# Kernel tuning notes

Hardware: AMD Instinct MI355X
Metric: run time of the kernel (lower is better)

Reference implementation:

```python
import jax, jax.numpy as jnp
import numpy as np

EMB = 1024   # emb_dim
HID = 1024   # hid_dim (must equal EMB for the original router to be well-formed)
E = 16       # num_experts
K = 2        # num_active_experts


def setup_inputs() -> dict:
    key = jax.random.key(0)
    ks = jax.random.split(key, 5)
    s_in = (2.0 / EMB) ** 0.5
    s_hid = (2.0 / HID) ** 0.5
    x = jax.random.normal(ks[0], (2, 4096, EMB), dtype=jnp.float32)
    w_gate = jax.random.normal(ks[1], (EMB, E), dtype=jnp.float32) * s_in
    w1 = jax.random.normal(ks[2], (E, EMB, HID), dtype=jnp.float32) * s_in  # exp_1 weights
    w2 = jax.random.normal(ks[3], (E, EMB, HID), dtype=jnp.float32) * s_in  # exp_2 weights
    wc = jax.random.normal(ks[4], (E, HID, EMB), dtype=jnp.float32) * s_hid  # contr weights
    return {"x": x, "w_gate": w_gate, "w1": w1, "w2": w2, "wc": wc}


def reference(x, w_gate, w1, w2, wc):
    b, s, d = x.shape
    xf = x.reshape(-1, d)                      # [N, d]
    n = xf.shape[0]
    # Router: softmax over expert logits, then top-k (no renormalization of topk scores,
    # matching the torch module).
    probs = jax.nn.softmax(xf @ w_gate, axis=-1)   # [N, E]
    scores, idx = jax.lax.top_k(probs, K)          # [N, K]
    # Dense gate matrix: gate[t, e] = score if e in topk(t) else 0 (topk indices distinct).
    gates = jnp.zeros((n, E), dtype=xf.dtype).at[jnp.arange(n)[:, None], idx].set(scores)
    # Loop (scan) over the fixed expert count; each expert runs a SwiGLU MLP over all
    # tokens and its output is combined with the (mostly zero) gate weights. This is the
    # standard dense-combine MoE reference: same math as the masked torch loop since
    # unselected tokens get gate 0.
    def body(acc, ws):
        w1e, w2e, wce, ge = ws                 # [d,h], [d,h], [h,d], [N]
        h = jax.nn.silu(xf @ w1e) * (xf @ w2e)  # [N, h]
        return acc + ge[:, None] * (h @ wce), None

    out, _ = jax.lax.scan(body, jnp.zeros_like(xf), (w1, w2, wc, gates.T))
    return out.reshape(b, s, d)
```

## Files before the change

kernel.cpp:

```cpp
#include <hip/hip_runtime.h>
#include <hip/hip_bf16.h>
#include <stdint.h>

#define EMB 1024
#define HID 1024
#define NE 16
#define NTOK 8192
#define NSLOT (NTOK * 2)
#define BM 128
#define BN 128
#define BK 32

typedef __bf16 bf16;
typedef __bf16 bf16x8 __attribute__((ext_vector_type(8)));
typedef __bf16 bf16x4 __attribute__((ext_vector_type(4)));
typedef float f32x4 __attribute__((ext_vector_type(4)));

#define GLOAD16(g, l)                                                        \
  __builtin_amdgcn_global_load_lds(                                          \
      (const __attribute__((address_space(1))) void*)(g),                    \
      (__attribute__((address_space(3))) void*)(l), 16, 0, 0)

__global__ void transpose_cvt3(const float* __restrict__ w1, const float* __restrict__ w2,
                               const float* __restrict__ wcs, bf16* __restrict__ w1t,
                               bf16* __restrict__ w2t, bf16* __restrict__ wct) {
  __shared__ float tile[32][33];
  int zz = blockIdx.z;
  const float* s; bf16* d;
  if (zz < 16)      { s = w1;  d = w1t; }
  else if (zz < 32) { s = w2;  d = w2t; }
  else              { s = wcs; d = wct; }
  int z = zz & 15;
  int x0 = blockIdx.x << 5, y0 = blockIdx.y << 5;
  s += (size_t)z * EMB * HID;
  d += (size_t)z * EMB * HID;
  int tx = threadIdx.x, ty = threadIdx.y;
#pragma unroll
  for (int i = 0; i < 32; i += 8)
    tile[ty + i][tx] = s[(size_t)(y0 + ty + i) * 1024 + x0 + tx];
  __syncthreads();
#pragma unroll
  for (int i = 0; i < 32; i += 8)
    d[(size_t)(x0 + ty + i) * 1024 + y0 + tx] = (bf16)tile[tx][ty + i];
}

__global__ void wgT_k(const float* __restrict__ wg, float* __restrict__ wgT) {
  int f = blockIdx.x * 256 + threadIdx.x;
  int d = f >> 4, e = f & 15;
  wgT[e * 1024 + d] = wg[f];
}

__launch_bounds__(1024)
__global__ void router_k(const float* __restrict__ x, const float* __restrict__ wgT,
                         bf16* __restrict__ xb,
                         int* __restrict__ tokexp, float* __restrict__ tokgate) {
  __shared__ float wgs[NE * 1024];
  for (int i = threadIdx.x; i < 4096; i += 1024)
    ((float4*)wgs)[i] = ((const float4*)wgT)[i];
  __syncthreads();

  int t = blockIdx.x * 16 + (threadIdx.x >> 6);
  int lane = threadIdx.x & 63;
  const float* xr = x + (size_t)t * EMB;

  float acc[NE];
#pragma unroll
  for (int e = 0; e < NE; e++) acc[e] = 0.f;

#pragma unroll
  for (int c = 0; c < 4; c++) {
    float4 xv = ((const float4*)xr)[c * 64 + lane];
    int dbase = c * 256 + lane * 4;
    bf16x4 o;
    o[0] = (bf16)xv.x; o[1] = (bf16)xv.y; o[2] = (bf16)xv.z; o[3] = (bf16)xv.w;
    *(bf16x4*)(xb + (size_t)t * EMB + dbase) = o;
#pragma unroll
    for (int e = 0; e < NE; e++) {
      float4 wv = *(const float4*)&wgs[e * 1024 + dbase];
      acc[e] += xv.x * wv.x + xv.y * wv.y + xv.z * wv.z + xv.w * wv.w;
    }
  }
#pragma unroll
  for (int e = 0; e < NE; e++) {
#pragma unroll
    for (int s = 32; s > 0; s >>= 1) acc[e] += __shfl_xor(acc[e], s);
  }
  if (lane == 0) {
    float m = acc[0];
#pragma unroll
    for (int e = 1; e < NE; e++) m = fmaxf(m, acc[e]);
    float p[NE]; float sum = 0.f;
#pragma unroll
    for (int e = 0; e < NE; e++) { p[e] = __expf(acc[e] - m); sum += p[e]; }
    float inv = 1.f / sum;
#pragma unroll
    for (int e = 0; e < NE; e++) p[e] *= inv;
    int i1 = 0;
#pragma unroll
    for (int e = 1; e < NE; e++) if (p[e] > p[i1]) i1 = e;
    int i2 = (i1 == 0) ? 1 : 0;
#pragma unroll
    for (int e = 0; e < NE; e++) if (e != i1 && p[e] > p[i2]) i2 = e;
    tokexp[2 * t] = i1; tokexp[2 * t + 1] = i2;
    tokgate[2 * t] = p[i1]; tokgate[2 * t + 1] = p[i2];
  }
}

__global__ void hist_k(const int* __restrict__ tokexp, int* __restrict__ blockcnt) {
  __shared__ int h[NE];
  int tid = threadIdx.x;
  if (tid < NE) h[tid] = 0;
  __syncthreads();
  int e = tokexp[blockIdx.x * 256 + tid];
  atomicAdd(&h[e], 1);
  __syncthreads();
  if (tid < NE) blockcnt[blockIdx.x * NE + tid] = h[tid];
}

__global__ void scan_k(const int* __restrict__ blockcnt, int* __restrict__ cnt,
                       int* __restrict__ eoff, int* __restrict__ blockoff) {
  __shared__ int scnt[NE], soff[NE];
  int t = threadIdx.x;
  if (t < NE) {
    int s = 0;
    for (int b = 0; b < 64; b++) s += blockcnt[b * NE + t];
    scnt[t] = s;
    cnt[t] = s;
  }
  __syncthreads();
  if (t == 0) {
    int s = 0;
    for (int e = 0; e < NE; e++) { soff[e] = s; eoff[e] = s; s += scnt[e]; }
  }
  __syncthreads();
  if (t < NE) {
    int run = soff[t];
    for (int b = 0; b < 64; b++) { blockoff[b * NE + t] = run; run += blockcnt[b * NE + t]; }
  }
}

__global__ void assign_k(const int* __restrict__ tokexp, const float* __restrict__ tokgate,
                         const int* __restrict__ blockoff, int* __restrict__ rowtok,
                         float* __restrict__ rowgate) {
  __shared__ int wavecnt[4][NE];
  __shared__ int waveoff[4][NE];
  int tid = threadIdx.x;
  int w = tid >> 6, lane = tid & 63;
  int s = blockIdx.x * 256 + tid;
  int e = tokexp[s];
  int rank = 0;
  unsigned long long ltmask = (1ull << lane) - 1ull;
#pragma unroll
  for (int ee = 0; ee < NE; ee++) {
    unsigned long long bal = __ballot(e == ee);
    if (e == ee) rank = __popcll(bal & ltmask);
    if (lane == ee) wavecnt[w][ee] = __popcll(bal);
  }
  __syncthreads();
  if (tid < 64) {
    int ww = tid >> 4, ee = tid & 15;
    int off = 0;
    for (int p = 0; p < ww; p++) off += wavecnt[p][ee];
    waveoff[ww][ee] = off;
  }
  __syncthreads();
  int pos = blockoff[blockIdx.x * NE + e] + waveoff[w][e] + rank;
  rowtok[pos] = s >> 1;
  rowgate[pos] = tokgate[s];
}

__launch_bounds__(256, 2)
__global__ void gemm1_k(const bf16* __restrict__ xb, const bf16* __restrict__ w1t,
                        const bf16* __restrict__ w2t, const int* __restrict__ cnt,
                        const int* __restrict__ eoff, const int* __restrict__ rowtok,
                        bf16* __restrict__ H) {
  int id = blockIdx.x;
  int nid = (id & 7) * 1024 + (id >> 3);
  int e = nid >> 9;
  int rem = nid & 511;
  int m0 = (rem >> 3) * BM;
  int n0 = (rem & 7) * BN;
  int n_e = cnt[e];
  if (m0 >= n_e) return;
  int base = eoff[e];

  __shared__ __align__(16) bf16 sA[BM * BK];
  __shared__ __align__(16) bf16 sB1[BN * BK];
  __shared__ __align__(16) bf16 sB2[BN * BK];

  int tid = threadIdx.x;
  int lane = tid & 63;
  int w = tid >> 6;
  int wr = (w >> 1) << 6;
  int wc = (w & 1) << 6;

  int srow = tid >> 2;
  int kc = (tid & 3) << 3;

  const bf16* ag[2];
#pragma unroll
  for (int i = 0; i < 2; i++) {
    int gi = base + m0 + (i << 6) + srow;
    gi = gi < NSLOT ? gi : NSLOT - 1;
    ag[i] = xb + (size_t)rowtok[gi] * EMB + kc;
  }
  const bf16* b1g = w1t + ((size_t)e * HID + n0 + srow) * EMB + kc;
  const bf16* b2g = w2t + ((size_t)e * HID + n0 + srow) * EMB + kc;

  char* lA = (char*)sA + w * 1024;
  char* lB1 = (char*)sB1 + w * 1024;
  char* lB2 = (char*)sB2 + w * 1024;

  f32x4 acc1[4][4] = {};
  f32x4 acc2[4][4] = {};

  int ra = (wr + (lane & 15)) * BK + ((lane >> 4) << 3);
  int rb = (wc + (lane & 15)) * BK + ((lane >> 4) << 3);

  for (int k0 = 0; k0 < EMB; k0 += BK) {
    GLOAD16(ag[0] + k0, lA);
    GLOAD16(ag[1] + k0, lA + 4096);
    GLOAD16(b1g + k0, lB1);
    GLOAD16(b1g + (size_t)64 * EMB + k0, lB1 + 4096);
    GLOAD16(b2g + k0, lB2);
    GLOAD16(b2g + (size_t)64 * EMB + k0, lB2 + 4096);
    __syncthreads();

    bf16x8 af[4], b1f[4], b2f[4];
#pragma unroll
    for (int m = 0; m < 4; m++) af[m] = *(const bf16x8*)&sA[ra + m * 16 * BK];
#pragma unroll
    for (int n = 0; n < 4; n++) {
      b1f[n] = *(const bf16x8*)&sB1[rb + n * 16 * BK];
      b2f[n] = *(const bf16x8*)&sB2[rb + n * 16 * BK];
    }
#pragma unroll
    for (int m = 0; m < 4; m++)
#pragma unroll
      for (int n = 0; n < 4; n++) {
        acc1[m][n] = __builtin_amdgcn_mfma_f32_16x16x32_bf16(af[m], b1f[n], acc1[m][n], 0, 0, 0);
        acc2[m][n] = __builtin_amdgcn_mfma_f32_16x16x32_bf16(af[m], b2f[n], acc2[m][n], 0, 0, 0);
      }
    __syncthreads();
  }

  int rf = wr + ((lane >> 4) << 2);
  int cf = n0 + wc + (lane & 15);
#pragma unroll
  for (int m = 0; m < 4; m++) {
#pragma unroll
    for (int n = 0; n < 4; n++) {
#pragma unroll
      for (int b = 0; b < 4; b++) {
        int gr = m0 + rf + m * 16 + b;
        if (gr < n_e) {
          float c1 = acc1[m][n][b];
          float c2 = acc2[m][n][b];
          float h = c1 * c2 / (1.f + __expf(-c1));
          H[(size_t)(base + gr) * HID + cf + n * 16] = (bf16)h;
        }
      }
    }
  }
}

__launch_bounds__(256, 2)
__global__ void gemm2_k(const bf16* __restrict__ H, const bf16* __restrict__ wct,
                        const int* __restrict__ cnt, const int* __restrict__ eoff,
                        const int* __restrict__ rowtok, const float* __restrict__ rowgate,
                        float* __restrict__ out) {
  int id = blockIdx.x;
  int nid = (id & 7) * 1024 + (id >> 3);
  int e = nid >> 9;
  int rem = nid & 511;
  int m0 = (rem >> 3) * BM;
  int n0 = (rem & 7) * BN;
  int n_e = cnt[e];
  if (m0 >= n_e) return;
  int base = eoff[e];

  __shared__ __align__(16) bf16 sA[BM * BK];
  __shared__ __align__(16) bf16 sB[BN * BK];

  int tid = threadIdx.x;
  int lane = tid & 63;
  int w = tid >> 6;
  int wr = (w >> 1) << 6;
  int wc = (w & 1) << 6;

  int srow = tid >> 2;
  int kc = (tid & 3) << 3;

  const bf16* ag[2];
#pragma unroll
  for (int i = 0; i < 2; i++) {
    int gi = base + m0 + (i << 6) + srow;
    gi = gi < NSLOT ? gi : NSLOT - 1;
    ag[i] = H + (size_t)gi * HID + kc;
  }
  const bf16* bg = wct + ((size_t)e * EMB + n0 + srow) * HID + kc;

  char* lA = (char*)sA + w * 1024;
  char* lB = (char*)sB + w * 1024;

  f32x4 acc[4][4] = {};

  int ra = (wr + (lane & 15)) * BK + ((lane >> 4) << 3);
  int rb = (wc + (lane & 15)) * BK + ((lane >> 4) << 3);

  for (int k0 = 0; k0 < HID; k0 += BK) {
    GLOAD16(ag[0] + k0, lA);
    GLOAD16(ag[1] + k0, lA + 4096);
    GLOAD16(bg + k0, lB);
    GLOAD16(bg + (size_t)64 * HID + k0, lB + 4096);
    __syncthreads();

    bf16x8 af[4], bfr[4];
#pragma unroll
    for (int m = 0; m < 4; m++) af[m] = *(const bf16x8*)&sA[ra + m * 16 * BK];
#pragma unroll
    for (int n = 0; n < 4; n++) bfr[n] = *(const bf16x8*)&sB[rb + n * 16 * BK];
#pragma unroll
    for (int m = 0; m < 4; m++)
#pragma unroll
      for (int n = 0; n < 4; n++)
        acc[m][n] = __builtin_amdgcn_mfma_f32_16x16x32_bf16(af[m], bfr[n], acc[m][n], 0, 0, 0);
    __syncthreads();
  }

  int rf = wr + ((lane >> 4) << 2);
  int cf = n0 + wc + (lane & 15);
#pragma unroll
  for (int m = 0; m < 4; m++) {
#pragma unroll
    for (int b = 0; b < 4; b++) {
      int gr = m0 + rf + m * 16 + b;
      if (gr < n_e) {
        int idx = base + gr;
        int tok = rowtok[idx];
        float g = rowgate[idx];
        float* orow = out + (size_t)tok * EMB + cf;
#pragma unroll
        for (int n = 0; n < 4; n++)
          atomicAdd(orow + n * 16, g * acc[m][n][b]);
      }
    }
  }
}

extern "C" void kernel_launch(void* const* d_in, const int* in_sizes, int n_in,
                              void* d_out, int out_size, void* d_ws, size_t ws_size,
                              hipStream_t stream) {
  const float* x  = (const float*)d_in[0];
  const float* wg = (const float*)d_in[1];
  const float* w1 = (const float*)d_in[2];
  const float* w2 = (const float*)d_in[3];
  const float* wc = (const float*)d_in[4];
  float* out = (float*)d_out;

  const size_t WELEM = (size_t)NE * EMB * HID;
  bf16* w1t  = (bf16*)d_ws;
  bf16* w2t  = w1t + WELEM;
  bf16* wct  = w2t + WELEM;
  bf16* xb   = wct + WELEM;
  bf16* Hbuf = xb + (size_t)NTOK * EMB;
  int* cnt      = (int*)(Hbuf + (size_t)NSLOT * HID);
  int* eoff     = cnt + 16;
  int* blockcnt = eoff + 16;
  int* blockoff = blockcnt + 64 * 16;
  int* tokexp   = blockoff + 64 * 16;
  float* tokgate = (float*)(tokexp + NSLOT);
  int* rowtok    = (int*)(tokgate + NSLOT);
  float* rowgate = (float*)(rowtok + NSLOT);
  float* wgT     = rowgate + NSLOT;

  hipMemsetAsync(out, 0, (size_t)out_size * sizeof(float), stream);

  dim3 tb(32, 8), tg(32, 32, 48);
  transpose_cvt3<<<tg, tb, 0, stream>>>(w1, w2, wc, w1t, w2t, wct);
  wgT_k<<<64, 256, 0, stream>>>(wg, wgT);
  router_k<<<NTOK / 16, 1024, 0, stream>>>(x, wgT, xb, tokexp, tokgate);
  hist_k<<<NSLOT / 256, 256, 0, stream>>>(tokexp, blockcnt);
  scan_k<<<1, 64, 0, stream>>>(blockcnt, cnt, eoff, blockoff);
  assign_k<<<NSLOT / 256, 256, 0, stream>>>(tokexp, tokgate, blockoff, rowtok, rowgate);
  gemm1_k<<<8192, 256, 0, stream>>>(xb, w1t, w2t, cnt, eoff, rowtok, Hbuf);
  gemm2_k<<<8192, 256, 0, stream>>>(Hbuf, wct, cnt, eoff, rowtok, rowgate, out);
}
```

Baseline: 308.9 us.

## Rewrite expert GEMMs with 256x256 tiles, double-buffered pipelining and interleaved gate/up weights

Both expert GEMMs move to 512-thread blocks with 256x256 output tiles and BK=64. K-tiles are double-buffered in 128KB of dynamic LDS with an XOR-swizzled layout, and the loop uses explicit vmcnt waits, barriers and setprio phases to overlap global loads with MFMA work. W1 and W2 are interleaved row-wise into one concatenated weight, so a single accumulator set yields both projections, and SwiGLU is formed by exchanging neighbouring lanes with a shuffle. gemm2 adds a 2-way split-K, relying on the existing atomic adds. The transpose/convert kernel is rewritten with 64x64 tiles and vectorized bf16 stores. The larger tiles cut redundant weight and activation traffic, but they waste more work on partially filled expert tiles, lower occupancy, and double the atomic traffic in gemm2.

Result: slower. 363.4 us (+17.6%).

```diff
diff --git a/kernel.cpp b/kernel.cpp
--- a/kernel.cpp
+++ b/kernel.cpp
@@ -7,9 +7,6 @@
 #define NE 16
 #define NTOK 8192
 #define NSLOT (NTOK * 2)
-#define BM 128
-#define BN 128
-#define BK 32
 
 typedef __bf16 bf16;
 typedef __bf16 bf16x8 __attribute__((ext_vector_type(8)));
@@ -21,27 +18,103 @@
       (const __attribute__((address_space(1))) void*)(g),                    \
       (__attribute__((address_space(3))) void*)(l), 16, 0, 0)
 
+
+#define VMW(N) asm volatile("s_waitcnt vmcnt(" #N ")" ::: "memory")
+#define NOPS ((void)0)
+
+#define PH_PRE                                                \
+  __builtin_amdgcn_s_barrier();                               \
+  asm volatile("s_waitcnt lgkmcnt(0)" ::: "memory");          \
+  __builtin_amdgcn_sched_barrier(0);                          \
+  __builtin_amdgcn_s_setprio(1)
+#define PH_POST                                               \
+  __builtin_amdgcn_s_setprio(0);                              \
+  __builtin_amdgcn_s_barrier()
+
+#define LDA(D, M, CK) (*(const bf16x8*)&sh[((((D)<<1) + wm) << 13) + l15 * 64 + (CK) + (M) * 1024])
+#define LDB(D, N, CK) (*(const bf16x8*)&sh[32768 + ((((D)<<1) + (wn >> 1)) << 13) + ((wn & 1) << 12) + l15 * 64 + (CK) + (N) * 1024])
+
+#define STG_A(D, KO) do {                                                     \
+    GLOAD16(agp00 + (KO), (char*)sh + ((((D)<<1) + 0) << 14) + wb);           \
+    GLOAD16(agp01 + (KO), (char*)sh + ((((D)<<1) + 0) << 14) + 8192 + wb);    \
+    GLOAD16(agp10 + (KO), (char*)sh + ((((D)<<1) + 1) << 14) + wb);           \
+    GLOAD16(agp11 + (KO), (char*)sh + ((((D)<<1) + 1) << 14) + 8192 + wb);    \
+  } while (0)
+#define STG_B(D, KO) do {                                                     \
+    GLOAD16(bgp00 + (KO), (char*)sh + 65536 + ((((D)<<1) + 0) << 14) + wb);   \
+    GLOAD16(bgp01 + (KO), (char*)sh + 65536 + ((((D)<<1) + 0) << 14) + 8192 + wb); \
+    GLOAD16(bgp10 + (KO), (char*)sh + 65536 + ((((D)<<1) + 1) << 14) + wb);   \
+    GLOAD16(bgp11 + (KO), (char*)sh + 65536 + ((((D)<<1) + 1) << 14) + 8192 + wb); \
+  } while (0)
+
+#define MM(MB, FA, FB) do {                                                   \
+    _Pragma("unroll") for (int mq = 0; mq < 4; mq++)                          \
+    _Pragma("unroll") for (int nq = 0; nq < 4; nq++)                          \
+      acc[(MB) + mq][nq] = __builtin_amdgcn_mfma_f32_16x16x32_bf16(           \
+          FA[mq], FB[nq], acc[(MB) + mq][nq], 0, 0, 0);                       \
+  } while (0)
+
+#define KTILE(D, S3, S4, W4) do {                                             \
+    bf16x8 fa[4], fb[4], g0[4], g1[4];                                        \
+    _Pragma("unroll") for (int q = 0; q < 4; q++) g0[q] = LDB(D, q, c0);      \
+    _Pragma("unroll") for (int q = 0; q < 4; q++) fa[q] = LDA(D, q, c0);      \
+    PH_PRE; MM(0, fa, g0); PH_POST;                                           \
+    _Pragma("unroll") for (int q = 0; q < 4; q++) fb[q] = LDA(D, 4 + q, c0);  \
+    _Pragma("unroll") for (int q = 0; q < 4; q++) g1[q] = LDB(D, q, c1);      \
+    PH_PRE; MM(4, fb, g0); PH_POST;                                           \
+    _Pragma("unroll") for (int q = 0; q < 4; q++) fa[q] = LDA(D, q, c1);      \
+    _Pragma("unroll") for (int q = 0; q < 4; q++) fb[q] = LDA(D, 4 + q, c1);  \
+    S3;                                                                       \
+    PH_PRE; MM(0, fa, g1); PH_POST;                                           \
+    S4; W4;                                                                   \
+    PH_PRE; MM(4, fb, g1); PH_POST;                                           \
+  } while (0)
+
+#define KLOOP(NT2) do {                                                       \
+    STG_A(0, 0); STG_B(0, 0); STG_A(1, 64); STG_B(1, 64);                     \
+    VMW(8); __builtin_amdgcn_s_barrier();                                     \
+    _Pragma("unroll 1") for (int i = 0; i < (NT2) - 1; i++) {                 \
+      int k2 = (i * 2 + 2) * 64, k3 = (i * 2 + 3) * 64;                       \
+      KTILE(0, STG_B(0, k2), STG_A(0, k2), VMW(6));                           \
+      KTILE(1, STG_B(1, k3), STG_A(1, k3), VMW(6));                           \
+    }                                                                         \
+    KTILE(0, NOPS, NOPS, VMW(0));                                             \
+    KTILE(1, NOPS, NOPS, NOPS);                                               \
+  } while (0)
+
 __global__ void transpose_cvt3(const float* __restrict__ w1, const float* __restrict__ w2,
-                               const float* __restrict__ wcs, bf16* __restrict__ w1t,
-                               bf16* __restrict__ w2t, bf16* __restrict__ wct) {
-  __shared__ float tile[32][33];
+                               const float* __restrict__ wcs, bf16* __restrict__ wcat,
+                               bf16* __restrict__ wct) {
+  __shared__ bf16 tile[64][68];
   int zz = blockIdx.z;
-  const float* s; bf16* d;
-  if (zz < 16)      { s = w1;  d = w1t; }
-  else if (zz < 32) { s = w2;  d = w2t; }
-  else              { s = wcs; d = wct; }
-  int z = zz & 15;
-  int x0 = blockIdx.x << 5, y0 = blockIdx.y << 5;
-  s += (size_t)z * EMB * HID;
-  d += (size_t)z * EMB * HID;
-  int tx = threadIdx.x, ty = threadIdx.y;
-#pragma unroll
-  for (int i = 0; i < 32; i += 8)
-    tile[ty + i][tx] = s[(size_t)(y0 + ty + i) * 1024 + x0 + tx];
-  __syncthreads();
-#pragma unroll
-  for (int i = 0; i < 32; i += 8)
-    d[(size_t)(x0 + ty + i) * 1024 + y0 + tx] = (bf16)tile[tx][ty + i];
+  const float* s; bf16* d; int mul, add;
+  if (zz < 16)      { s = w1 + ((size_t)zz << 20);        d = wcat + ((size_t)zz << 21);        mul = 2; add = 0; }
+  else if (zz < 32) { s = w2 + ((size_t)(zz - 16) << 20); d = wcat + ((size_t)(zz - 16) << 21); mul = 2; add = 1; }
+  else              { s = wcs + ((size_t)(zz - 32) << 20); d = wct + ((size_t)(zz - 32) << 20); mul = 1; add = 0; }
+  int k0 = blockIdx.y << 6, n0 = blockIdx.x << 6;
+  int t = threadIdx.x;
+
+  int r = t >> 4, c4 = t & 15;
+#pragma unroll
+  for (int i = 0; i < 4; i++) {
+    int row = r + (i << 4);
+    float4 v = *(const float4*)&s[(size_t)(k0 + row) * 1024 + n0 + (c4 << 2)];
+    bf16x4 o;
+    o[0] = (bf16)v.x; o[1] = (bf16)v.y; o[2] = (bf16)v.z; o[3] = (bf16)v.w;
+    *(bf16x4*)&tile[row][c4 << 2] = o;
+  }
+  __syncthreads();
+
+  int r8 = t >> 3, ch = t & 7;
+#pragma unroll
+  for (int i = 0; i < 2; i++) {
+    int on = r8 + (i << 5);
+    bf16x8 v;
+#pragma unroll
+    for (int j = 0; j < 8; j++) v[j] = tile[(ch << 3) + j][on];
+    int orow = (n0 + on) * mul + add;
+    *(bf16x8*)&d[(size_t)orow * 1024 + k0 + (ch << 3)] = v;
+  }
 }
 
 __global__ void wgT_k(const float* __restrict__ wg, float* __restrict__ wgT) {
@@ -169,183 +242,126 @@
   rowgate[pos] = tokgate[s];
 }
 
-__launch_bounds__(256, 2)
-__global__ void gemm1_k(const bf16* __restrict__ xb, const bf16* __restrict__ w1t,
-                        const bf16* __restrict__ w2t, const int* __restrict__ cnt,
-                        const int* __restrict__ eoff, const int* __restrict__ rowtok,
-                        bf16* __restrict__ H) {
+__launch_bounds__(512, 2)
+__global__ void gemm1_k(const bf16* __restrict__ xb, const bf16* __restrict__ wcat,
+                        const int* __restrict__ cnt, const int* __restrict__ eoff,
+                        const int* __restrict__ rowtok, bf16* __restrict__ Hb) {
   int id = blockIdx.x;
-  int nid = (id & 7) * 1024 + (id >> 3);
-  int e = nid >> 9;
-  int rem = nid & 511;
-  int m0 = (rem >> 3) * BM;
-  int n0 = (rem & 7) * BN;
+  int nid = (id & 7) * 512 + (id >> 3);
+  int e = nid >> 8, rem = nid & 255;
+  int m0 = (rem >> 3) << 8, n0 = (rem & 7) << 8;
   int n_e = cnt[e];
   if (m0 >= n_e) return;
-  int base = eoff[e];
-
-  __shared__ __align__(16) bf16 sA[BM * BK];
-  __shared__ __align__(16) bf16 sB1[BN * BK];
-  __shared__ __align__(16) bf16 sB2[BN * BK];
-
-  int tid = threadIdx.x;
-  int lane = tid & 63;
-  int w = tid >> 6;
-  int wr = (w >> 1) << 6;
-  int wc = (w & 1) << 6;
-
-  int srow = tid >> 2;
-  int kc = (tid & 3) << 3;
-
-  const bf16* ag[2];
-#pragma unroll
-  for (int i = 0; i < 2; i++) {
-    int gi = base + m0 + (i << 6) + srow;
-    gi = gi < NSLOT ? gi : NSLOT - 1;
-    ag[i] = xb + (size_t)rowtok[gi] * EMB + kc;
-  }
-  const bf16* b1g = w1t + ((size_t)e * HID + n0 + srow) * EMB + kc;
-  const bf16* b2g = w2t + ((size_t)e * HID + n0 + srow) * EMB + kc;
-
-  char* lA = (char*)sA + w * 1024;
-  char* lB1 = (char*)sB1 + w * 1024;
-  char* lB2 = (char*)sB2 + w * 1024;
-
-  f32x4 acc1[4][4] = {};
-  f32x4 acc2[4][4] = {};
-
-  int ra = (wr + (lane & 15)) * BK + ((lane >> 4) << 3);
-  int rb = (wc + (lane & 15)) * BK + ((lane >> 4) << 3);
-
-  for (int k0 = 0; k0 < EMB; k0 += BK) {
-    GLOAD16(ag[0] + k0, lA);
-    GLOAD16(ag[1] + k0, lA + 4096);
-    GLOAD16(b1g + k0, lB1);
-    GLOAD16(b1g + (size_t)64 * EMB + k0, lB1 + 4096);
-    GLOAD16(b2g + k0, lB2);
-    GLOAD16(b2g + (size_t)64 * EMB + k0, lB2 + 4096);
-    __syncthreads();
-
-    bf16x8 af[4], b1f[4], b2f[4];
-#pragma unroll
-    for (int m = 0; m < 4; m++) af[m] = *(const bf16x8*)&sA[ra + m * 16 * BK];
-#pragma unroll
-    for (int n = 0; n < 4; n++) {
-      b1f[n] = *(const bf16x8*)&sB1[rb + n * 16 * BK];
-      b2f[n] = *(const bf16x8*)&sB2[rb + n * 16 * BK];
-    }
-#pragma unroll
-    for (int m = 0; m < 4; m++)
-#pragma unroll
-      for (int n = 0; n < 4; n++) {
-        acc1[m][n] = __builtin_amdgcn_mfma_f32_16x16x32_bf16(af[m], b1f[n], acc1[m][n], 0, 0, 0);
-        acc2[m][n] = __builtin_amdgcn_mfma_f32_16x16x32_bf16(af[m], b2f[n], acc2[m][n], 0, 0, 0);
-      }
-    __syncthreads();
-  }
-
-  int rf = wr + ((lane >> 4) << 2);
-  int cf = n0 + wc + (lane & 15);
-#pragma unroll
-  for (int m = 0; m < 4; m++) {
-#pragma unroll
-    for (int n = 0; n < 4; n++) {
+  int base0 = eoff[e];
+  extern __shared__ bf16 sh[];
+
+  int tid = threadIdx.x, lane = tid & 63, w = tid >> 6;
+  int wm = w >> 2, wn = w & 3;
+  int l15 = lane & 15, l4 = lane >> 4, r7 = l15 & 7;
+  int c0 = ((l4 ^ r7) << 3), c1 = (((4 + l4) ^ r7) << 3);
+  int srow = tid >> 3;
+  int kg8 = (((tid & 7) ^ (srow & 7)) << 3);
+  int wb = w << 10;
+
+  const bf16 *agp00, *agp01, *agp10, *agp11, *bgp00, *bgp01, *bgp10, *bgp11;
+  {
+    int g0 = base0 + m0 + srow;        g0 = g0 < NSLOT ? g0 : NSLOT - 1;
+    int g1 = base0 + m0 + 64 + srow;   g1 = g1 < NSLOT ? g1 : NSLOT - 1;
+    int g2 = base0 + m0 + 128 + srow;  g2 = g2 < NSLOT ? g2 : NSLOT - 1;
+    int g3 = base0 + m0 + 192 + srow;  g3 = g3 < NSLOT ? g3 : NSLOT - 1;
+    agp00 = xb + ((size_t)rowtok[g0] << 10) + kg8;
+    agp01 = xb + ((size_t)rowtok[g1] << 10) + kg8;
+    agp10 = xb + ((size_t)rowtok[g2] << 10) + kg8;
+    agp11 = xb + ((size_t)rowtok[g3] << 10) + kg8;
+    const bf16* wce = wcat + ((size_t)e << 21);
+    bgp00 = wce + ((size_t)(n0 + srow) << 10) + kg8;
+    bgp01 = wce + ((size_t)(n0 + 64 + srow) << 10) + kg8;
+    bgp10 = wce + ((size_t)(n0 + 128 + srow) << 10) + kg8;
+    bgp11 = wce + ((size_t)(n0 + 192 + srow) << 10) + kg8;
+  }
+
+  f32x4 acc[8][4] = {};
+  KLOOP(8);
+
+  int rb0 = m0 + (wm << 7) + (l4 << 2);
+  int cb0 = n0 + (wn << 6) + l15;
+#pragma unroll
+  for (int m = 0; m < 8; m++)
+#pragma unroll
+    for (int n = 0; n < 4; n++)
 #pragma unroll
       for (int b = 0; b < 4; b++) {
-        int gr = m0 + rf + m * 16 + b;
-        if (gr < n_e) {
-          float c1 = acc1[m][n][b];
-          float c2 = acc2[m][n][b];
-          float h = c1 * c2 / (1.f + __expf(-c1));
-          H[(size_t)(base + gr) * HID + cf + n * 16] = (bf16)h;
+        float v = acc[m][n][b];
+        float p = __shfl_xor(v, 1);
+        int gr = rb0 + m * 16 + b;
+        if (!(l15 & 1) && gr < n_e) {
+          float h = v * p / (1.f + __expf(-v));
+          Hb[((size_t)(base0 + gr) << 10) + ((cb0 + n * 16) >> 1)] = (bf16)h;
         }
       }
-    }
-  }
-}
-
-__launch_bounds__(256, 2)
-__global__ void gemm2_k(const bf16* __restrict__ H, const bf16* __restrict__ wct,
+}
+
+__launch_bounds__(512, 2)
+__global__ void gemm2_k(const bf16* __restrict__ Hb, const bf16* __restrict__ wct,
                         const int* __restrict__ cnt, const int* __restrict__ eoff,
                         const int* __restrict__ rowtok, const float* __restrict__ rowgate,
                         float* __restrict__ out) {
   int id = blockIdx.x;
-  int nid = (id & 7) * 1024 + (id >> 3);
-  int e = nid >> 9;
-  int rem = nid & 511;
-  int m0 = (rem >> 3) * BM;
-  int n0 = (rem & 7) * BN;
+  int nid = (id & 7) * 512 + (id >> 3);
+  int e = nid >> 8, rem = nid & 255;
+  int m0 = (rem >> 3) << 8;
+  int n0 = ((rem >> 1) & 3) << 8;
+  int ks = (rem & 1) << 9;
   int n_e = cnt[e];
   if (m0 >= n_e) return;
-  int base = eoff[e];
-
-  __shared__ __align__(16) bf16 sA[BM * BK];
-  __shared__ __align__(16) bf16 sB[BN * BK];
-
-  int tid = threadIdx.x;
-  int lane = tid & 63;
-  int w = tid >> 6;
-  int wr = (w >> 1) << 6;
-  int wc = (w & 1) << 6;
-
-  int srow = tid >> 2;
-  int kc = (tid & 3) << 3;
-
-  const bf16* ag[2];
-#pragma unroll
-  for (int i = 0; i < 2; i++) {
-    int gi = base + m0 + (i << 6) + srow;
-    gi = gi < NSLOT ? gi : NSLOT - 1;
-    ag[i] = H + (size_t)gi * HID + kc;
-  }
-  const bf16* bg = wct + ((size_t)e * EMB + n0 + srow) * HID + kc;
-
-  char* lA = (char*)sA + w * 1024;
-  char* lB = (char*)sB + w * 1024;
-
-  f32x4 acc[4][4] = {};
-
-  int ra = (wr + (lane & 15)) * BK + ((lane >> 4) << 3);
-  int rb = (wc + (lane & 15)) * BK + ((lane >> 4) << 3);
-
-  for (int k0 = 0; k0 < HID; k0 += BK) {
-    GLOAD16(ag[0] + k0, lA);
-    GLOAD16(ag[1] + k0, lA + 4096);
-    GLOAD16(bg + k0, lB);
-    GLOAD16(bg + (size_t)64 * HID + k0, lB + 4096);
-    __syncthreads();
-
-    bf16x8 af[4], bfr[4];
-#pragma unroll
-    for (int m = 0; m < 4; m++) af[m] = *(const bf16x8*)&sA[ra + m * 16 * BK];
-#pragma unroll
-    for (int n = 0; n < 4; n++) bfr[n] = *(const bf16x8*)&sB[rb + n * 16 * BK];
-#pragma unroll
-    for (int m = 0; m < 4; m++)
-#pragma unroll
-      for (int n = 0; n < 4; n++)
-        acc[m][n] = __builtin_amdgcn_mfma_f32_16x16x32_bf16(af[m], bfr[n], acc[m][n], 0, 0, 0);
-    __syncthreads();
-  }
-
-  int rf = wr + ((lane >> 4) << 2);
-  int cf = n0 + wc + (lane & 15);
-#pragma unroll
-  for (int m = 0; m < 4; m++) {
+  int base0 = eoff[e];
+  extern __shared__ bf16 sh[];
+
+  int tid = threadIdx.x, lane = tid & 63, w = tid >> 6;
+  int wm = w >> 2, wn = w & 3;
+  int l15 = lane & 15, l4 = lane >> 4, r7 = l15 & 7;
+  int c0 = ((l4 ^ r7) << 3), c1 = (((4 + l4) ^ r7) << 3);
+  int srow = tid >> 3;
+  int kg8 = (((tid & 7) ^ (srow & 7)) << 3);
+  int wb = w << 10;
+
+  const bf16 *agp00, *agp01, *agp10, *agp11, *bgp00, *bgp01, *bgp10, *bgp11;
+  {
+    int g0 = base0 + m0 + srow;        g0 = g0 < NSLOT ? g0 : NSLOT - 1;
+    int g1 = base0 + m0 + 64 + srow;   g1 = g1 < NSLOT ? g1 : NSLOT - 1;
+    int g2 = base0 + m0 + 128 + srow;  g2 = g2 < NSLOT ? g2 : NSLOT - 1;
+    int g3 = base0 + m0 + 192 + srow;  g3 = g3 < NSLOT ? g3 : NSLOT - 1;
+    agp00 = Hb + ((size_t)g0 << 10) + ks + kg8;
+    agp01 = Hb + ((size_t)g1 << 10) + ks + kg8;
+    agp10 = Hb + ((size_t)g2 << 10) + ks + kg8;
+    agp11 = Hb + ((size_t)g3 << 10) + ks + kg8;
+    const bf16* wce = wct + ((size_t)e << 20);
+    bgp00 = wce + ((size_t)(n0 + srow) << 10) + ks + kg8;
+    bgp01 = wce + ((size_t)(n0 + 64 + srow) << 10) + ks + kg8;
+    bgp10 = wce + ((size_t)(n0 + 128 + srow) << 10) + ks + kg8;
+    bgp11 = wce + ((size_t)(n0 + 192 + srow) << 10) + ks + kg8;
+  }
+
+  f32x4 acc[8][4] = {};
+  KLOOP(4);
+
+  int rb0 = m0 + (wm << 7) + (l4 << 2);
+  int cb0 = n0 + (wn << 6) + l15;
+#pragma unroll
+  for (int m = 0; m < 8; m++)
 #pragma unroll
     for (int b = 0; b < 4; b++) {
-      int gr = m0 + rf + m * 16 + b;
+      int gr = rb0 + m * 16 + b;
       if (gr < n_e) {
-        int idx = base + gr;
+        int idx = base0 + gr;
         int tok = rowtok[idx];
         float g = rowgate[idx];
-        float* orow = out + (size_t)tok * EMB + cf;
+        float* orow = out + ((size_t)tok << 10) + cb0;
 #pragma unroll
         for (int n = 0; n < 4; n++)
           atomicAdd(orow + n * 16, g * acc[m][n][b]);
       }
     }
-  }
 }
 
 extern "C" void kernel_launch(void* const* d_in, const int* in_sizes, int n_in,
@@ -358,13 +374,11 @@
   const float* wc = (const float*)d_in[4];
   float* out = (float*)d_out;
 
-  const size_t WELEM = (size_t)NE * EMB * HID;
-  bf16* w1t  = (bf16*)d_ws;
-  bf16* w2t  = w1t + WELEM;
-  bf16* wct  = w2t + WELEM;
-  bf16* xb   = wct + WELEM;
-  bf16* Hbuf = xb + (size_t)NTOK * EMB;
-  int* cnt      = (int*)(Hbuf + (size_t)NSLOT * HID);
+  bf16* wcat = (bf16*)d_ws;
+  bf16* wct  = wcat + ((size_t)NE << 21);
+  bf16* xb   = wct + ((size_t)NE << 20);
+  bf16* Hb   = xb + ((size_t)NTOK << 10);
+  int* cnt      = (int*)(Hb + ((size_t)NSLOT << 10));
   int* eoff     = cnt + 16;
   int* blockcnt = eoff + 16;
   int* blockoff = blockcnt + 64 * 16;
@@ -374,15 +388,18 @@
   float* rowgate = (float*)(rowtok + NSLOT);
   float* wgT     = rowgate + NSLOT;
 
+  hipFuncSetAttribute((const void*)gemm1_k, hipFuncAttributeMaxDynamicSharedMemorySize, 131072);
+  hipFuncSetAttribute((const void*)gemm2_k, hipFuncAttributeMaxDynamicSharedMemorySize, 131072);
+
   hipMemsetAsync(out, 0, (size_t)out_size * sizeof(float), stream);
 
-  dim3 tb(32, 8), tg(32, 32, 48);
-  transpose_cvt3<<<tg, tb, 0, stream>>>(w1, w2, wc, w1t, w2t, wct);
+  dim3 tg(16, 16, 48);
+  transpose_cvt3<<<tg, 256, 0, stream>>>(w1, w2, wc, wcat, wct);
   wgT_k<<<64, 256, 0, stream>>>(wg, wgT);
   router_k<<<NTOK / 16, 1024, 0, stream>>>(x, wgT, xb, tokexp, tokgate);
   hist_k<<<NSLOT / 256, 256, 0, stream>>>(tokexp, blockcnt);
   scan_k<<<1, 64, 0, stream>>>(blockcnt, cnt, eoff, blockoff);
   assign_k<<<NSLOT / 256, 256, 0, stream>>>(tokexp, tokgate, blockoff, rowtok, rowgate);
-  gemm1_k<<<8192, 256, 0, stream>>>(xb, w1t, w2t, cnt, eoff, rowtok, Hbuf);
-  gemm2_k<<<8192, 256, 0, stream>>>(Hbuf, wct, cnt, eoff, rowtok, rowgate, out);
-}
+  gemm1_k<<<4096, 512, 131072, stream>>>(xb, wcat, cnt, eoff, rowtok, Hb);
+  gemm2_k<<<4096, 512, 131072, stream>>>(Hb, wct, cnt, eoff, rowtok, rowgate, out);
+}
```
